# Performance work log

Hardware: AMD Instinct MI355X
Metric: run time of the kernel (lower is better)

The kernel has to match this reference:

```python
import jax, jax.numpy as jnp
import numpy as np

B, T, C, H = 2, 2048, 1024, 16
HD = C // H
HID = C * 4 // 3  # 1365, SwiGLU hidden
EPS = 1e-5


def _ln(x, g, b):
    m = x.mean(-1, keepdims=True)
    v = ((x - m) ** 2).mean(-1, keepdims=True)
    return (x - m) / jnp.sqrt(v + EPS) * g + b


def setup_inputs() -> dict:
    key0 = jax.random.key(0)
    ks = jax.random.split(key0, 16)
    s = 0.02
    inp = {
        'query': jax.random.normal(ks[0], (B, T, C), jnp.float32),
        'key': jax.random.normal(ks[1], (B, T, C), jnp.float32),
        'g_q': jnp.ones((C,), jnp.float32), 'b_q': jnp.zeros((C,), jnp.float32),
        'g_k': jnp.ones((C,), jnp.float32), 'b_k': jnp.zeros((C,), jnp.float32),
        'in_proj_w': jax.random.normal(ks[2], (3 * C, C), jnp.float32) * s,
        'in_proj_b': jnp.zeros((3 * C,), jnp.float32),
        'out_w': jax.random.normal(ks[3], (C, C), jnp.float32) * s,
        'out_b': jnp.zeros((C,), jnp.float32),
        'proj_w': jax.random.normal(ks[4], (C, C), jnp.float32) * s,
        'proj_b': jnp.zeros((C,), jnp.float32),
        'rel_table': jax.random.normal(ks[5], (H, 2 * 2048 - 1), jnp.float32) * s,
        'g_ffn': jnp.ones((C,), jnp.float32), 'b_ffn': jnp.zeros((C,), jnp.float32),
        'w1': jax.random.normal(ks[6], (HID, C), jnp.float32) * s,
        'w2': jax.random.normal(ks[7], (HID, C), jnp.float32) * s,
        'w3': jax.random.normal(ks[8], (C, HID), jnp.float32) * s,
        'g_out': jnp.ones((C,), jnp.float32), 'b_out': jnp.zeros((C,), jnp.float32),
        'max_len': 2048,
    }
    return inp


def reference(query, key, g_q, b_q, g_k, b_k, in_proj_w, in_proj_b, out_w, out_b,
              proj_w, proj_b, rel_table, g_ffn, b_ffn, w1, w2, w3, g_out, b_out, max_len):
    Tq, Tk = query.shape[1], key.shape[1]
    q = _ln(query, g_q, b_q)
    k = _ln(key, g_k, b_k)
    # in-projection (torch MHA packed weights)
    wq, wk, wv = jnp.split(in_proj_w, 3, axis=0)
    bq, bk, bv = jnp.split(in_proj_b, 3, axis=0)
    qp = (q @ wq.T + bq).reshape(B, Tq, H, HD).transpose(0, 2, 1, 3)
    kp = (k @ wk.T + bk).reshape(B, Tk, H, HD).transpose(0, 2, 1, 3)
    vp = (k @ wv.T + bv).reshape(B, Tk, H, HD).transpose(0, 2, 1, 3)
    # relative-position bias, mean over heads -> [Tq,Tk] additive mask
    rel_idx = jnp.clip(jnp.arange(Tq)[:, None] - jnp.arange(Tk)[None, :] + (max_len - 1),
                       0, 2 * max_len - 2)
    mask = rel_table[:, rel_idx].mean(axis=0)  # [Tq,Tk]
    scores = jnp.einsum('bhqd,bhkd->bhqk', qp, kp) / jnp.sqrt(jnp.float32(HD))
    attn = jax.nn.softmax(scores + mask[None, None], axis=-1)
    ctx = jnp.einsum('bhqk,bhkd->bhqd', attn, vp)
    ctx = ctx.transpose(0, 2, 1, 3).reshape(B, Tq, C)
    attn_out = ctx @ out_w.T + out_b
    attn_out = attn_out @ proj_w.T + proj_b
    x = query + attn_out
    # SwiGLU FFN (proj dropout/dropout are identity at eval)
    h = _ln(x, g_ffn, b_ffn)
    ff = (jax.nn.silu(h @ w1.T) * (h @ w2.T)) @ w3.T
    x = x + ff
    return _ln(x, g_out, b_out)
```

## Files before the change

kernel.cpp:

```cpp
#include <hip/hip_runtime.h>
#include <hip/hip_bf16.h>

static constexpr int Bb  = 2;
static constexpr int Tt  = 2048;
static constexpr int Cc  = 1024;
static constexpr int Hh  = 16;
static constexpr int HDi = 64;
static constexpr int HID = 1365;
static constexpr int HIDP = 1408;
static constexpr int Mm  = Bb * Tt;

typedef unsigned short u16;
typedef __attribute__((ext_vector_type(8))) short bf16x8;
typedef __attribute__((ext_vector_type(4))) float f32x4;
typedef __attribute__((ext_vector_type(8))) unsigned short u16x8;
typedef __attribute__((ext_vector_type(4))) unsigned short u16x4;

__device__ inline u16 f2bf(float f) {
    unsigned u = __builtin_bit_cast(unsigned, f);
    u += 0x7fffu + ((u >> 16) & 1u);
    return (u16)(u >> 16);
}

__device__ inline unsigned cvtpk(float lo, float hi) {
    unsigned r;
    asm("v_cvt_pk_bf16_f32 %0, %1, %2" : "=v"(r) : "v"(lo), "v"(hi));
    return r;
}

__device__ inline float vexp2(float x) {
    float r;
    asm("v_exp_f32 %0, %1" : "=v"(r) : "v"(x));
    return r;
}

__device__ inline void gl16(const void* g, void* l) {
    __builtin_amdgcn_global_load_lds(
        (const __attribute__((address_space(1))) unsigned*)g,
        (__attribute__((address_space(3))) unsigned*)l, 16, 0, 0);
}

template<int OUTBF>
__global__ __launch_bounds__(256) void ln_k(const float* __restrict__ x,
                                            const float* __restrict__ g,
                                            const float* __restrict__ b,
                                            void* __restrict__ yv) {
    int row = blockIdx.x;
    int tid = threadIdx.x;
    const float4* xr = (const float4*)(x + (size_t)row * Cc);
    float4 v = xr[tid];
    float s  = v.x + v.y + v.z + v.w;
    float ss = v.x*v.x + v.y*v.y + v.z*v.z + v.w*v.w;
    __shared__ float rs[256], rq[256];
    rs[tid] = s; rq[tid] = ss;
    __syncthreads();
    for (int o = 128; o > 0; o >>= 1) {
        if (tid < o) { rs[tid] += rs[tid+o]; rq[tid] += rq[tid+o]; }
        __syncthreads();
    }
    float mean = rs[0] * (1.f/Cc);
    float var  = rq[0] * (1.f/Cc) - mean*mean;
    float inv  = rsqrtf(var + 1e-5f);
    float4 gv = ((const float4*)g)[tid];
    float4 bv = ((const float4*)b)[tid];
    float o0 = (v.x-mean)*inv*gv.x + bv.x;
    float o1 = (v.y-mean)*inv*gv.y + bv.y;
    float o2 = (v.z-mean)*inv*gv.z + bv.z;
    float o3 = (v.w-mean)*inv*gv.w + bv.w;
    if (OUTBF) {
        u16x4 o4 = { f2bf(o0), f2bf(o1), f2bf(o2), f2bf(o3) };
        ((u16x4*)((u16*)yv + (size_t)row * Cc))[tid] = o4;
    } else {
        float4 o4 = { o0, o1, o2, o3 };
        ((float4*)((float*)yv + (size_t)row * Cc))[tid] = o4;
    }
}

__global__ __launch_bounds__(256) void prepln_k(const float* __restrict__ query,
                                                const float* __restrict__ key,
                                                const float* __restrict__ gq, const float* __restrict__ bq,
                                                const float* __restrict__ gk, const float* __restrict__ bk,
                                                u16* __restrict__ qn, u16* __restrict__ kn,
                                                const float* __restrict__ in_proj_w, u16* __restrict__ wA,
                                                const float* __restrict__ proj_w,  u16* __restrict__ wPb,
                                                const float* __restrict__ w1, u16* __restrict__ w1b,
                                                const float* __restrict__ w2, u16* __restrict__ w2b,
                                                const float* __restrict__ w3, u16* __restrict__ w3b,
                                                const float* __restrict__ out_w, u16* __restrict__ wOt,
                                                const float* __restrict__ out_b, const float* __restrict__ bp,
                                                float* __restrict__ bc,
                                                const float* __restrict__ rel, float* __restrict__ mr) {
    __shared__ float sh[64*65];
    int bid = blockIdx.x, tid = threadIdx.x;
    if (bid < 2*Mm) {
        const float* x; const float* g; const float* bb; u16* y; int r;
        if (bid < Mm) { x = query; g = gq; bb = bq; y = qn; r = bid; }
        else          { x = key;   g = gk; bb = bk; y = kn; r = bid - Mm; }
        float4 v = ((const float4*)(x + (size_t)r * Cc))[tid];
        float s  = v.x + v.y + v.z + v.w;
        float ss = v.x*v.x + v.y*v.y + v.z*v.z + v.w*v.w;
        float* rs = sh; float* rq2 = sh + 256;
        rs[tid] = s; rq2[tid] = ss;
        __syncthreads();
        for (int o = 128; o > 0; o >>= 1) {
            if (tid < o) { rs[tid] += rs[tid+o]; rq2[tid] += rq2[tid+o]; }
            __syncthreads();
        }
        float mean = rs[0] * (1.f/Cc);
        float var  = rq2[0] * (1.f/Cc) - mean*mean;
        float inv  = rsqrtf(var + 1e-5f);
        float4 gv = ((const float4*)g)[tid];
        float4 bv = ((const float4*)bb)[tid];
        u16x4 o4 = { f2bf((v.x-mean)*inv*gv.x + bv.x), f2bf((v.y-mean)*inv*gv.y + bv.y),
                     f2bf((v.z-mean)*inv*gv.z + bv.z), f2bf((v.w-mean)*inv*gv.w + bv.w) };
        ((u16x4*)(y + (size_t)r * Cc))[tid] = o4;
        return;
    }
    bid -= 2*Mm;
    if (bid < 3456) {
        int u = bid * 256 + tid;
        const float* src; u16* dst; int valid;
        if (u < 1536*256)                   { src = in_proj_w; dst = wA;  valid = 3*Cc*Cc; }
        else if ((u -= 1536*256) < 512*256) { src = proj_w;    dst = wPb; valid = Cc*Cc; }
        else if ((u -= 512*256) < 704*256)  { src = w1;        dst = w1b; valid = HID*Cc; }
        else     { u -= 704*256;              src = w2;        dst = w2b; valid = HID*Cc; }
        int e0 = u * 8;
        u16x8 o;
        if (e0 + 8 <= valid) {
            float4 a = *(const float4*)(src + e0);
            float4 b = *(const float4*)(src + e0 + 4);
            o[0]=f2bf(a.x); o[1]=f2bf(a.y); o[2]=f2bf(a.z); o[3]=f2bf(a.w);
            o[4]=f2bf(b.x); o[5]=f2bf(b.y); o[6]=f2bf(b.z); o[7]=f2bf(b.w);
        } else {
            #pragma unroll
            for (int j = 0; j < 8; j++) { int e = e0 + j; o[j] = f2bf(e < valid ? src[e] : 0.f); }
        }
        *(u16x8*)(dst + (size_t)e0) = o;
    } else if (bid < 4160) {
        int idx = (bid - 3456) * 256 + tid;
        int e0 = idx * 8;
        int r = e0 / HIDP, c0 = e0 - r * HIDP;
        u16x8 o;
        #pragma unroll
        for (int j = 0; j < 8; j++) {
            int c = c0 + j;
            o[j] = f2bf(c < HID ? w3[(size_t)r * HID + c] : 0.f);
        }
        *(u16x8*)(w3b + (size_t)e0) = o;
    } else if (bid < 4416) {
        int id = bid - 4160;
        int j0 = (id & 15) * 64, c0 = (id >> 4) * 64;
        #pragma unroll
        for (int i = 0; i < 16; i++) {
            int e = tid + i*256;
            int c = e >> 6, j = e & 63;
            sh[c*65 + j] = out_w[(size_t)(c0 + c) * Cc + j0 + j];
        }
        __syncthreads();
        #pragma unroll
        for (int i = 0; i < 16; i++) {
            int e = tid + i*256;
            int j = e >> 6, c = e & 63;
            wOt[(size_t)(j0 + j) * Cc + c0 + c] = f2bf(sh[c*65 + j]);
        }
    } else if (bid < 5440) {
        int i = bid - 4416;
        float4 w = ((const float4*)(proj_w + (size_t)i * Cc))[tid];
        float4 b = ((const float4*)out_b)[tid];
        float s = w.x*b.x + w.y*b.y + w.z*b.z + w.w*b.w;
        sh[tid] = s; __syncthreads();
        for (int o = 128; o > 0; o >>= 1) {
            if (tid < o) sh[tid] += sh[tid+o];
            __syncthreads();
        }
        if (tid == 0) bc[i] = sh[0] + bp[i];
    } else {
        int j = (bid - 5440) * 256 + tid;
        if (j < 2*Tt - 1) {
            float s = 0.f;
            #pragma unroll
            for (int h = 0; h < Hh; h++) s += rel[(size_t)h * (2*Tt - 1) + j];
            mr[j] = s * (1.f/Hh);
        }
    }
}

template<int OUTBF, int HASRES, int HASBIAS>
__global__ __launch_bounds__(256) void mgemm64_k(const u16* __restrict__ A,
                                                 const u16* __restrict__ W,
                                                 const float* __restrict__ bias,
                                                 const float* __restrict__ res,
                                                 void* __restrict__ outv,
                                                 int N, int K) {
    __shared__ u16 As[2][64*32];
    __shared__ u16 Ws[2][128*32];
    int bm = blockIdx.y * 64, bn = blockIdx.x * 128;
    int tid = threadIdx.x, w = tid >> 6, l = tid & 63;
    int lr = l & 15, lh = l >> 4;
    int wm = (w >> 1) * 32, wn = (w & 1) * 64;
    f32x4 acc[2][4] = {};

    auto stage = [&](int buf, int kt) {
        {
            int row = tid >> 2, slot = tid & 3;
            int ko = kt + ((slot ^ (row & 3)) << 3);
            gl16(A + (size_t)(bm + row) * K + ko, (char*)As[buf] + tid * 16);
        }
        #pragma unroll
        for (int c = 0; c < 2; c++) {
            int i = c*256 + tid;
            int row = i >> 2, slot = i & 3;
            int ko = kt + ((slot ^ (row & 3)) << 3);
            gl16(W + (size_t)(bn + row) * K + ko, (char*)Ws[buf] + (c*256 + tid) * 16);
        }
    };
    stage(0, 0);
    for (int kt = 0; kt < K; kt += 32) {
        int buf = (kt >> 5) & 1;
        __syncthreads();
        if (kt + 32 < K) stage(buf ^ 1, kt + 32);
        bf16x8 af[2], wf[4];
        #pragma unroll
        for (int f = 0; f < 2; f++) {
            int r = wm + f*16 + lr;
            af[f] = *(const bf16x8*)((const char*)As[buf] + r*64 + ((lh ^ (r & 3)) << 4));
        }
        #pragma unroll
        for (int f = 0; f < 4; f++) {
            int rn = wn + f*16 + lr;
            wf[f] = *(const bf16x8*)((const char*)Ws[buf] + rn*64 + ((lh ^ (rn & 3)) << 4));
        }
        #pragma unroll
        for (int fm = 0; fm < 2; fm++)
            #pragma unroll
            for (int fn = 0; fn < 4; fn++)
                acc[fm][fn] = __builtin_amdgcn_mfma_f32_16x16x32_bf16(af[fm], wf[fn], acc[fm][fn], 0, 0, 0);
    }

    #pragma unroll
    for (int fm = 0; fm < 2; fm++) {
        #pragma unroll
        for (int r = 0; r < 4; r++) {
            int row = bm + wm + fm*16 + lh*4 + r;
            #pragma unroll
            for (int fn = 0; fn < 4; fn++) {
                int col = bn + wn + fn*16 + lr;
                float v = acc[fm][fn][r];
                if (HASBIAS) v += bias[col];
                if (HASRES)  v += res[(size_t)row * N + col];
                if (OUTBF) ((u16*)outv)[(size_t)row * N + col] = f2bf(v);
                else       ((float*)outv)[(size_t)row * N + col] = v;
            }
        }
    }
}

__global__ __launch_bounds__(256) void mqkv_k(const u16* __restrict__ qn,
                                              const u16* __restrict__ kn,
                                              const u16* __restrict__ wA,
                                              const float* __restrict__ bias3,
                                              u16* __restrict__ out3,
                                              const u16* __restrict__ wPb,
                                              const u16* __restrict__ wOt,
                                              u16* __restrict__ wCb) {
    __shared__ u16 As[2][64*32];
    __shared__ u16 Ws[2][128*32];

    int bid = blockIdx.x;
    int xcd = bid & 7, j = bid >> 3;
    int p = xcd * 26 + (j >> 3), x = j & 7;
    const u16* A; const u16* W; const float* bias = bias3; u16* out;
    int bm, bn = x * 128, hasb;
    if (p < 192) {
        int z = p >> 6, y = p & 63;
        A = z ? kn : qn; W = wA + (size_t)z * Cc * Cc;
        bias = bias3 + z * Cc; out = out3 + (size_t)z * Mm * Cc;
        bm = y * 64; hasb = 1;
    } else {
        A = wPb; W = wOt; out = wCb;
        bm = (p - 192) * 64; hasb = 0;
    }

    int tid = threadIdx.x, w = tid >> 6, l = tid & 63;
    int lr = l & 15, lh = l >> 4;
    int wm = (w >> 1) * 32, wn = (w & 1) * 64;
    f32x4 acc[2][4] = {};

    auto stage = [&](int buf, int kt) {
        {
            int row = tid >> 2, slot = tid & 3;
            int ko = kt + ((slot ^ (row & 3)) << 3);
            gl16(A + (size_t)(bm + row) * Cc + ko, (char*)As[buf] + tid * 16);
        }
        #pragma unroll
        for (int c = 0; c < 2; c++) {
            int i = c*256 + tid;
            int row = i >> 2, slot = i & 3;
            int ko = kt + ((slot ^ (row & 3)) << 3);
            gl16(W + (size_t)(bn + row) * Cc + ko, (char*)Ws[buf] + (c*256 + tid) * 16);
        }
    };
    stage(0, 0);
    for (int kt = 0; kt < Cc; kt += 32) {
        int buf = (kt >> 5) & 1;
        __syncthreads();
        if (kt + 32 < Cc) stage(buf ^ 1, kt + 32);
        bf16x8 af[2], wf[4];
        #pragma unroll
        for (int f = 0; f < 2; f++) {
            int r = wm + f*16 + lr;
            af[f] = *(const bf16x8*)((const char*)As[buf] + r*64 + ((lh ^ (r & 3)) << 4));
        }
        #pragma unroll
        for (int f = 0; f < 4; f++) {
            int rn = wn + f*16 + lr;
            wf[f] = *(const bf16x8*)((const char*)Ws[buf] + rn*64 + ((lh ^ (rn & 3)) << 4));
        }
        #pragma unroll
        for (int fm = 0; fm < 2; fm++)
            #pragma unroll
            for (int fn = 0; fn < 4; fn++)
                acc[fm][fn] = __builtin_amdgcn_mfma_f32_16x16x32_bf16(af[fm], wf[fn], acc[fm][fn], 0, 0, 0);
    }

    #pragma unroll
    for (int fm = 0; fm < 2; fm++) {
        #pragma unroll
        for (int r = 0; r < 4; r++) {
            int orow = bm + wm + fm*16 + lh*4 + r;
            #pragma unroll
            for (int fn = 0; fn < 4; fn++) {
                int col = bn + wn + fn*16 + lr;
                float v = acc[fm][fn][r];
                if (hasb) v += bias[col];
                out[(size_t)orow * Cc + col] = f2bf(v);
            }
        }
    }
}

__global__ __launch_bounds__(256) void mswiglu64_k(const u16* __restrict__ A,
                                                   const u16* __restrict__ W1,
                                                   const u16* __restrict__ W2,
                                                   u16* __restrict__ out,
                                                   int N, int K) {
    __shared__ u16 As[2][64*32];
    __shared__ u16 W1s[2][128*32];
    __shared__ u16 W2s[2][128*32];
    int bm = blockIdx.y * 64, bn = blockIdx.x * 128;
    int tid = threadIdx.x, w = tid >> 6, l = tid & 63;
    int lr = l & 15, lh = l >> 4;
    int wm = (w >> 1) * 32, wn = (w & 1) * 64;
    f32x4 acc1[2][4] = {};
    f32x4 acc2[2][4] = {};

    auto stage = [&](int buf, int kt) {
        {
            int row = tid >> 2, slot = tid & 3;
            int ko = kt + ((slot ^ (row & 3)) << 3);
            gl16(A + (size_t)(bm + row) * K + ko, (char*)As[buf] + tid * 16);
        }
        #pragma unroll
        for (int c = 0; c < 2; c++) {
            int i = c*256 + tid;
            int row = i >> 2, slot = i & 3;
            int ko = kt + ((slot ^ (row & 3)) << 3);
            gl16(W1 + (size_t)(bn + row) * K + ko, (char*)W1s[buf] + (c*256 + tid) * 16);
            gl16(W2 + (size_t)(bn + row) * K + ko, (char*)W2s[buf] + (c*256 + tid) * 16);
        }
    };
    stage(0, 0);
    for (int kt = 0; kt < K; kt += 32) {
        int buf = (kt >> 5) & 1;
        __syncthreads();
        if (kt + 32 < K) stage(buf ^ 1, kt + 32);
        bf16x8 af[2], w1f[4], w2f[4];
        #pragma unroll
        for (int f = 0; f < 2; f++) {
            int r = wm + f*16 + lr;
            af[f] = *(const bf16x8*)((const char*)As[buf] + r*64 + ((lh ^ (r & 3)) << 4));
        }
        #pragma unroll
        for (int f = 0; f < 4; f++) {
            int rn = wn + f*16 + lr;
            int offn = rn*64 + ((lh ^ (rn & 3)) << 4);
            w1f[f] = *(const bf16x8*)((const char*)W1s[buf] + offn);
            w2f[f] = *(const bf16x8*)((const char*)W2s[buf] + offn);
        }
        #pragma unroll
        for (int fm = 0; fm < 2; fm++)
            #pragma unroll
            for (int fn = 0; fn < 4; fn++) {
                acc1[fm][fn] = __builtin_amdgcn_mfma_f32_16x16x32_bf16(af[fm], w1f[fn], acc1[fm][fn], 0, 0, 0);
                acc2[fm][fn] = __builtin_amdgcn_mfma_f32_16x16x32_bf16(af[fm], w2f[fn], acc2[fm][fn], 0, 0, 0);
            }
    }

    #pragma unroll
    for (int fm = 0; fm < 2; fm++) {
        #pragma unroll
        for (int r = 0; r < 4; r++) {
            int row = bm + wm + fm*16 + lh*4 + r;
            #pragma unroll
            for (int fn = 0; fn < 4; fn++) {
                int col = bn + wn + fn*16 + lr;
                float a = acc1[fm][fn][r];
                float sig = 1.f / (1.f + __expf(-a));
                out[(size_t)row * N + col] = f2bf(a * sig * acc2[fm][fn][r]);
            }
        }
    }
}

__global__ __launch_bounds__(256) void vt_k(const u16* __restrict__ vp,
                                            u16* __restrict__ vt) {
    int blk = blockIdx.x;
    int bh = blk >> 5, kb = blk & 31;
    int b = bh >> 4, h = bh & 15;
    __shared__ u16 t[64][65];
    int tid = threadIdx.x;
    size_t bc = (size_t)b*Tt*Cc + (size_t)h*HDi;
    #pragma unroll
    for (int i = 0; i < 16; i++) {
        int e = tid + i*256;
        int k = e >> 6, d = e & 63;
        t[d][k] = vp[bc + (size_t)(kb*64 + k)*Cc + d];
    }
    __syncthreads();
    #pragma unroll
    for (int i = 0; i < 16; i++) {
        int e = tid + i*256;
        int d = e >> 6, k = e & 63;
        vt[((size_t)bh*64 + d)*Tt + kb*64 + k] = t[d][k];
    }
}

__global__ __launch_bounds__(512) void fattn_k(const u16* __restrict__ qp,
                                               const u16* __restrict__ kp,
                                               const u16* __restrict__ vt,
                                               const float* __restrict__ mr,
                                               u16* __restrict__ ctx) {
    __shared__ alignas(128) u16 Kt[2*8192];
    __shared__ alignas(128) u16 Vts[2*8192];
    __shared__ float mrw[2176];

    constexpr float C1 = 0.18033688011118324f;

    int bid = blockIdx.x;
    int blk = ((bid & 7) << 6) | (bid >> 3);
    int qt = blk & 15, h = (blk >> 4) & 15, b = blk >> 8;
    int q0 = qt * 128;
    int tid = threadIdx.x, w = tid >> 6, l = tid & 63;
    int lr = l & 15, lh = l >> 4;
    size_t bc = (size_t)b * Tt * Cc + (size_t)h * HDi;
    const u16* vtb = vt + (size_t)(b*Hh + h) * HDi * Tt;

    for (int i = tid; i < 2175; i += 512) mrw[i] = mr[q0 + i] * 8.f;

    bf16x8 qa[2];
    {
        const u16* qrow = qp + bc + (size_t)(q0 + w*16 + lr) * Cc;
        qa[0] = *(const bf16x8*)(qrow + lh*8);
        qa[1] = *(const bf16x8*)(qrow + 32 + lh*8);
    }

    f32x4 oacc[4] = {};
    float mrun = -1e30f, lrun = 0.f;

    const char* pKb0 = (const char*)Kt + (lr>>2)*1024 + (lr&3)*128
                       + ((lh ^ (lr & 3)) << 4) + (((lr >> 2) & 1) << 6);
    const char* pKb1 = (const char*)((size_t)pKb0 ^ 64);
    int cr2 = lr >> 2;
    const char* pVb = (const char*)Vts + lr*256 + ((lh ^ (lr & 3)) << 4);
    const char* pVc0 = pVb + (((0 ^ cr2) & 3) << 6);
    const char* pVc1 = pVb + (((1 ^ cr2) & 3) << 6);
    const char* pVc2 = pVb + (((2 ^ cr2) & 3) << 6);
    const char* pVc3 = pVb + (((3 ^ cr2) & 3) << 6);
    const char* pm = (const char*)mrw + (w*16 + lr - lh*8 + 2047 - 103) * 4;

    int ksl = tid & 7, kr0 = tid >> 3;
    int so_k = (ksl ^ (kr0 & 7) ^ (((kr0 >> 3) & 1) << 2)) << 3;
    const u16* gK = kp + bc + (size_t)kr0 * Cc + so_k;
    int vsl = tid & 15, vr0 = tid >> 4;
    int so_v = (vsl ^ (vr0 & 15)) << 3;
    const u16* gV = vtb + (size_t)vr0 * Tt + so_v;
    int wb = (tid & 448) * 16;
    char* dK0 = (char*)Kt  + wb;
    char* dV0 = (char*)Vts + wb;

    auto stage = [&](int bufo) {
        gl16(gK,                      dK0 + bufo);
        gl16(gK + (size_t)64*Cc,      dK0 + bufo + 8192);
        gl16(gV,                      dV0 + bufo);
        gl16(gV + (size_t)32*Tt,      dV0 + bufo + 8192);
        gK += 128*Cc;
        gV += 128;
    };

    auto tile = [&](int bufo) {
        f32x4 s[8];
        #pragma unroll
        for (int f = 0; f < 8; f++) {
            int ob = 103 - (f & 1)*32 - ((f >> 1) & 1)*4 - (f >> 2)*64;
            s[f][0] = *(const float*)(pm + (ob    ) * 4);
            s[f][1] = *(const float*)(pm + (ob - 1) * 4);
            s[f][2] = *(const float*)(pm + (ob - 2) * 4);
            s[f][3] = *(const float*)(pm + (ob - 3) * 4);
        }
        pm -= 512;
        __builtin_amdgcn_s_setprio(1);
        {
            const char* k0 = pKb0 + bufo;
            const char* k1 = pKb1 + bufo;
            bf16x8 kb;
            kb = *(const bf16x8*)(k0 + 0);     s[0] = __builtin_amdgcn_mfma_f32_16x16x32_bf16(kb, qa[0], s[0], 0, 0, 0);
            kb = *(const bf16x8*)(k1 + 0);     s[0] = __builtin_amdgcn_mfma_f32_16x16x32_bf16(kb, qa[1], s[0], 0, 0, 0);
            kb = *(const bf16x8*)(k0 + 4096);  s[1] = __builtin_amdgcn_mfma_f32_16x16x32_bf16(kb, qa[0], s[1], 0, 0, 0);
            kb = *(const bf16x8*)(k1 + 4096);  s[1] = __builtin_amdgcn_mfma_f32_16x16x32_bf16(kb, qa[1], s[1], 0, 0, 0);
            kb = *(const bf16x8*)(k1 + 512);   s[2] = __builtin_amdgcn_mfma_f32_16x16x32_bf16(kb, qa[0], s[2], 0, 0, 0);
            kb = *(const bf16x8*)(k0 + 512);   s[2] = __builtin_amdgcn_mfma_f32_16x16x32_bf16(kb, qa[1], s[2], 0, 0, 0);
            kb = *(const bf16x8*)(k1 + 4608);  s[3] = __builtin_amdgcn_mfma_f32_16x16x32_bf16(kb, qa[0], s[3], 0, 0, 0);
            kb = *(const bf16x8*)(k0 + 4608);  s[3] = __builtin_amdgcn_mfma_f32_16x16x32_bf16(kb, qa[1], s[3], 0, 0, 0);
            kb = *(const bf16x8*)(k0 + 8192);  s[4] = __builtin_amdgcn_mfma_f32_16x16x32_bf16(kb, qa[0], s[4], 0, 0, 0);
            kb = *(const bf16x8*)(k1 + 8192);  s[4] = __builtin_amdgcn_mfma_f32_16x16x32_bf16(kb, qa[1], s[4], 0, 0, 0);
            kb = *(const bf16x8*)(k0 + 12288); s[5] = __builtin_amdgcn_mfma_f32_16x16x32_bf16(kb, qa[0], s[5], 0, 0, 0);
            kb = *(const bf16x8*)(k1 + 12288); s[5] = __builtin_amdgcn_mfma_f32_16x16x32_bf16(kb, qa[1], s[5], 0, 0, 0);
            kb = *(const bf16x8*)(k1 + 8704);  s[6] = __builtin_amdgcn_mfma_f32_16x16x32_bf16(kb, qa[0], s[6], 0, 0, 0);
            kb = *(const bf16x8*)(k0 + 8704);  s[6] = __builtin_amdgcn_mfma_f32_16x16x32_bf16(kb, qa[1], s[6], 0, 0, 0);
            kb = *(const bf16x8*)(k1 + 12800); s[7] = __builtin_amdgcn_mfma_f32_16x16x32_bf16(kb, qa[0], s[7], 0, 0, 0);
            kb = *(const bf16x8*)(k0 + 12800); s[7] = __builtin_amdgcn_mfma_f32_16x16x32_bf16(kb, qa[1], s[7], 0, 0, 0);
        }
        __builtin_amdgcn_s_setprio(0);

        float tm = -1e30f;
        #pragma unroll
        for (int f = 0; f < 8; f++)
            #pragma unroll
            for (int r = 0; r < 4; r++) tm = fmaxf(tm, s[f][r]);
        tm = fmaxf(tm, __shfl_xor(tm, 16));
        tm = fmaxf(tm, __shfl_xor(tm, 32));

        float corr = 1.f;
        bool nod = __all(tm <= mrun + 64.f);
        if (!nod) {
            float mn = fmaxf(mrun, tm);
            corr = vexp2((mrun - mn) * C1);
            mrun = mn;
        }
        float mnc = mrun * C1;
        float ts = 0.f;
        #pragma unroll
        for (int f = 0; f < 8; f++)
            #pragma unroll
            for (int r = 0; r < 4; r++) {
                float e = vexp2(fmaf(s[f][r], C1, -mnc));
                s[f][r] = e; ts += e;
            }
        ts += __shfl_xor(ts, 16);
        ts += __shfl_xor(ts, 32);
        if (nod) {
            lrun += ts;
        } else {
            lrun = lrun*corr + ts;
            #pragma unroll
            for (int f = 0; f < 4; f++) {
                oacc[f][0] *= corr; oacc[f][1] *= corr;
                oacc[f][2] *= corr; oacc[f][3] *= corr;
            }
        }

        uint4 pb0u = { cvtpk(s[0][0], s[0][1]), cvtpk(s[0][2], s[0][3]),
                       cvtpk(s[2][0], s[2][1]), cvtpk(s[2][2], s[2][3]) };
        uint4 pb1u = { cvtpk(s[1][0], s[1][1]), cvtpk(s[1][2], s[1][3]),
                       cvtpk(s[3][0], s[3][1]), cvtpk(s[3][2], s[3][3]) };
        uint4 pb2u = { cvtpk(s[4][0], s[4][1]), cvtpk(s[4][2], s[4][3]),
                       cvtpk(s[6][0], s[6][1]), cvtpk(s[6][2], s[6][3]) };
        uint4 pb3u = { cvtpk(s[5][0], s[5][1]), cvtpk(s[5][2], s[5][3]),
                       cvtpk(s[7][0], s[7][1]), cvtpk(s[7][2], s[7][3]) };
        bf16x8 pb0 = __builtin_bit_cast(bf16x8, pb0u);
        bf16x8 pb1 = __builtin_bit_cast(bf16x8, pb1u);
        bf16x8 pb2 = __builtin_bit_cast(bf16x8, pb2u);
        bf16x8 pb3 = __builtin_bit_cast(bf16x8, pb3u);

        __builtin_amdgcn_s_setprio(1);
        #pragma unroll
        for (int ff = 0; ff < 4; ff++) {
            bf16x8 vb;
            vb = *(const bf16x8*)(pVc0 + bufo + ff*4096);
            oacc[ff] = __builtin_amdgcn_mfma_f32_16x16x32_bf16(vb, pb0, oacc[ff], 0, 0, 0);
            vb = *(const bf16x8*)(pVc1 + bufo + ff*4096);
            oacc[ff] = __builtin_amdgcn_mfma_f32_16x16x32_bf16(vb, pb1, oacc[ff], 0, 0, 0);
            vb = *(const bf16x8*)(pVc2 + bufo + ff*4096);
            oacc[ff] = __builtin_amdgcn_mfma_f32_16x16x32_bf16(vb, pb2, oacc[ff], 0, 0, 0);
            vb = *(const bf16x8*)(pVc3 + bufo + ff*4096);
            oacc[ff] = __builtin_amdgcn_mfma_f32_16x16x32_bf16(vb, pb3, oacc[ff], 0, 0, 0);
        }
        __builtin_amdgcn_s_setprio(0);
    };

    stage(0);
    #pragma unroll 1
    for (int kt = 0; kt < 16; kt += 2) {
        __syncthreads();
        stage(16384);
        tile(0);
        __syncthreads();
        if (kt < 14) stage(0);
        tile(16384);
    }

    float iv = 1.f / lrun;
    size_t rowoff = bc + (size_t)(q0 + w*16 + lr) * Cc;
    #pragma unroll
    for (int f = 0; f < 4; f++) {
        u16x4 o4 = { f2bf(oacc[f][0]*iv), f2bf(oacc[f][1]*iv),
                     f2bf(oacc[f][2]*iv), f2bf(oacc[f][3]*iv) };
        *(u16x4*)(ctx + rowoff + f*16 + lh*4) = o4;
    }
}

extern "C" void kernel_launch(void* const* d_in, const int* in_sizes, int n_in,
                              void* d_out, int out_size, void* d_ws, size_t ws_size,
                              hipStream_t stream) {
    const float* query     = (const float*)d_in[0];
    const float* key       = (const float*)d_in[1];
    const float* g_q       = (const float*)d_in[2];
    const float* b_q       = (const float*)d_in[3];
    const float* g_k       = (const float*)d_in[4];
    const float* b_k       = (const float*)d_in[5];
    const float* in_proj_w = (const float*)d_in[6];
    const float* in_proj_b = (const float*)d_in[7];
    const float* out_w     = (const float*)d_in[8];
    const float* out_b     = (const float*)d_in[9];
    const float* proj_w    = (const float*)d_in[10];
    const float* proj_b    = (const float*)d_in[11];
    const float* rel_table = (const float*)d_in[12];
    const float* g_ffn     = (const float*)d_in[13];
    const float* b_ffn     = (const float*)d_in[14];
    const float* w1        = (const float*)d_in[15];
    const float* w2        = (const float*)d_in[16];
    const float* w3        = (const float*)d_in[17];
    const float* g_out     = (const float*)d_in[18];
    const float* b_out     = (const float*)d_in[19];

    char* p = (char*)d_ws;
    auto alloc = [&](size_t bytes) { char* r = p; p += bytes; return r; };
    const size_t MCb = (size_t)Mm * Cc * 2;
    u16* wA  = (u16*)alloc((size_t)3*Cc*Cc*2);
    u16* wPb = (u16*)alloc((size_t)Cc*Cc*2);
    u16* wOt = (u16*)alloc((size_t)Cc*Cc*2);
    u16* wCb = (u16*)alloc((size_t)Cc*Cc*2);
    u16* w1b = (u16*)alloc((size_t)HIDP*Cc*2);
    u16* w2b = (u16*)alloc((size_t)HIDP*Cc*2);
    u16* w3b = (u16*)alloc((size_t)Cc*HIDP*2);
    float* bc = (float*)alloc(Cc*4);
    float* mr = (float*)alloc(4096*4);
    u16* qn = (u16*)alloc(MCb);
    u16* kn = (u16*)alloc(MCb);
    u16* qp = (u16*)alloc(MCb);
    u16* kp = (u16*)alloc(MCb);
    u16* vp = (u16*)alloc(MCb);
    u16* vt = (u16*)alloc(MCb);
    float* x  = (float*)alloc((size_t)Mm*Cc*4);
    float* x2 = (float*)alloc((size_t)Mm*Cc*4);
    u16* ctx = qn;
    u16* h   = qp;
    u16* gf  = vp;

    dim3 blk(256);
    prepln_k<<<2*Mm + 5456, blk, 0, stream>>>(query, key, g_q, b_q, g_k, b_k, qn, kn,
                                              in_proj_w, wA, proj_w, wPb, w1, w1b, w2, w2b,
                                              w3, w3b, out_w, wOt, out_b, proj_b, bc, rel_table, mr);

    mqkv_k<<<1664, blk, 0, stream>>>(qn, kn, wA, in_proj_b, qp, wPb, wOt, wCb);

    vt_k<<<Bb*Hh*32, blk, 0, stream>>>(vp, vt);
    fattn_k<<<Bb*Hh*16, dim3(512), 0, stream>>>(qp, kp, vt, mr, ctx);

    dim3 g1(Cc/128, Mm/64);
    mgemm64_k<0,1,1><<<g1, blk, 0, stream>>>(ctx, wCb, bc, query, x, Cc, Cc);

    ln_k<1><<<Mm, blk, 0, stream>>>(x, g_ffn, b_ffn, h);
    dim3 g2(HIDP/128, Mm/64);
    mswiglu64_k<<<g2, blk, 0, stream>>>(h, w1b, w2b, gf, HIDP, Cc);
    dim3 g3(Cc/128, Mm/64);
    mgemm64_k<0,1,0><<<g3, blk, 0, stream>>>(gf, w3b, nullptr, x, x2, Cc, HIDP);

    ln_k<0><<<Mm, blk, 0, stream>>>(x2, g_out, b_out, d_out);
}
```

Before: 241.2 us.

## Fuse V transpose into QKV GEMM epilogue and reorder softmax sum

The V-projection blocks of the QKV GEMM now stage their output tile through shared memory and write it directly in transposed [b,h,d,t] layout. This removes the separate vt_k kernel launch and the round trip of V through global memory. In the attention kernel, the row-max is computed with a tree reduction, and the row-sum of the probabilities is moved after the PV MFMAs so it can overlap with them. The fused path adds an extra LDS round trip and two barriers to a third of the GEMM blocks, and it makes the transposed stores strided.

```diff
diff --git a/kernel.cpp b/kernel.cpp
--- a/kernel.cpp
+++ b/kernel.cpp
@@ -262,20 +262,22 @@
                                               u16* __restrict__ out3,
                                               const u16* __restrict__ wPb,
                                               const u16* __restrict__ wOt,
-                                              u16* __restrict__ wCb) {
-    __shared__ u16 As[2][64*32];
-    __shared__ u16 Ws[2][128*32];
+                                              u16* __restrict__ wCb,
+                                              u16* __restrict__ vt) {
+    __shared__ char smem[24576];
+    char* AsB = smem;
+    char* WsB = smem + 8192;
 
     int bid = blockIdx.x;
     int xcd = bid & 7, j = bid >> 3;
     int p = xcd * 26 + (j >> 3), x = j & 7;
     const u16* A; const u16* W; const float* bias = bias3; u16* out;
-    int bm, bn = x * 128, hasb;
+    int bm, bn = x * 128, hasb, isv = 0;
     if (p < 192) {
         int z = p >> 6, y = p & 63;
         A = z ? kn : qn; W = wA + (size_t)z * Cc * Cc;
         bias = bias3 + z * Cc; out = out3 + (size_t)z * Mm * Cc;
-        bm = y * 64; hasb = 1;
+        bm = y * 64; hasb = 1; isv = (z == 2);
     } else {
         A = wPb; W = wOt; out = wCb;
         bm = (p - 192) * 64; hasb = 0;
@@ -290,14 +292,14 @@
         {
             int row = tid >> 2, slot = tid & 3;
             int ko = kt + ((slot ^ (row & 3)) << 3);
-            gl16(A + (size_t)(bm + row) * Cc + ko, (char*)As[buf] + tid * 16);
+            gl16(A + (size_t)(bm + row) * Cc + ko, AsB + buf*4096 + tid * 16);
         }
         #pragma unroll
         for (int c = 0; c < 2; c++) {
             int i = c*256 + tid;
             int row = i >> 2, slot = i & 3;
             int ko = kt + ((slot ^ (row & 3)) << 3);
-            gl16(W + (size_t)(bn + row) * Cc + ko, (char*)Ws[buf] + (c*256 + tid) * 16);
+            gl16(W + (size_t)(bn + row) * Cc + ko, WsB + buf*8192 + (c*256 + tid) * 16);
         }
     };
     stage(0, 0);
@@ -309,12 +311,12 @@
         #pragma unroll
         for (int f = 0; f < 2; f++) {
             int r = wm + f*16 + lr;
-            af[f] = *(const bf16x8*)((const char*)As[buf] + r*64 + ((lh ^ (r & 3)) << 4));
+            af[f] = *(const bf16x8*)(AsB + buf*4096 + r*64 + ((lh ^ (r & 3)) << 4));
         }
         #pragma unroll
         for (int f = 0; f < 4; f++) {
             int rn = wn + f*16 + lr;
-            wf[f] = *(const bf16x8*)((const char*)Ws[buf] + rn*64 + ((lh ^ (rn & 3)) << 4));
+            wf[f] = *(const bf16x8*)(WsB + buf*8192 + rn*64 + ((lh ^ (rn & 3)) << 4));
         }
         #pragma unroll
         for (int fm = 0; fm < 2; fm++)
@@ -323,18 +325,45 @@
                 acc[fm][fn] = __builtin_amdgcn_mfma_f32_16x16x32_bf16(af[fm], wf[fn], acc[fm][fn], 0, 0, 0);
     }
 
-    #pragma unroll
-    for (int fm = 0; fm < 2; fm++) {
-        #pragma unroll
-        for (int r = 0; r < 4; r++) {
-            int orow = bm + wm + fm*16 + lh*4 + r;
-            #pragma unroll
-            for (int fn = 0; fn < 4; fn++) {
-                int col = bn + wn + fn*16 + lr;
-                float v = acc[fm][fn][r];
-                if (hasb) v += bias[col];
-                out[(size_t)orow * Cc + col] = f2bf(v);
+    if (!isv) {
+        #pragma unroll
+        for (int fm = 0; fm < 2; fm++) {
+            #pragma unroll
+            for (int r = 0; r < 4; r++) {
+                int orow = bm + wm + fm*16 + lh*4 + r;
+                #pragma unroll
+                for (int fn = 0; fn < 4; fn++) {
+                    int col = bn + wn + fn*16 + lr;
+                    float v = acc[fm][fn][r];
+                    if (hasb) v += bias[col];
+                    out[(size_t)orow * Cc + col] = f2bf(v);
+                }
             }
+        }
+    } else {
+        __syncthreads();
+        u16* T = (u16*)smem;
+        #pragma unroll
+        for (int fm = 0; fm < 2; fm++)
+            #pragma unroll
+            for (int r = 0; r < 4; r++) {
+                int lt = wm + fm*16 + lh*4 + r;
+                #pragma unroll
+                for (int fn = 0; fn < 4; fn++) {
+                    int c = wn + fn*16 + lr;
+                    T[lt*130 + c] = f2bf(acc[fm][fn][r] + bias[bn + c]);
+                }
+            }
+        __syncthreads();
+        int b = bm >> 11, t0 = bm & 2047;
+        int h0 = bn >> 6;
+        #pragma unroll
+        for (int i = 0; i < 32; i++) {
+            int e = i*256 + tid;
+            int dcol = e >> 6, t = e & 63;
+            u16 v = T[t*130 + dcol];
+            int h = h0 + (dcol >> 6), d = dcol & 63;
+            vt[(size_t)((b*Hh + h)*HDi + d) * Tt + t0 + t] = v;
         }
     }
 }
@@ -409,29 +438,6 @@
                 out[(size_t)row * N + col] = f2bf(a * sig * acc2[fm][fn][r]);
             }
         }
-    }
-}
-
-__global__ __launch_bounds__(256) void vt_k(const u16* __restrict__ vp,
-                                            u16* __restrict__ vt) {
-    int blk = blockIdx.x;
-    int bh = blk >> 5, kb = blk & 31;
-    int b = bh >> 4, h = bh & 15;
-    __shared__ u16 t[64][65];
-    int tid = threadIdx.x;
-    size_t bc = (size_t)b*Tt*Cc + (size_t)h*HDi;
-    #pragma unroll
-    for (int i = 0; i < 16; i++) {
-        int e = tid + i*256;
-        int k = e >> 6, d = e & 63;
-        t[d][k] = vp[bc + (size_t)(kb*64 + k)*Cc + d];
-    }
-    __syncthreads();
-    #pragma unroll
-    for (int i = 0; i < 16; i++) {
-        int e = tid + i*256;
-        int d = e >> 6, k = e & 63;
-        vt[((size_t)bh*64 + d)*Tt + kb*64 + k] = t[d][k];
     }
 }
 
@@ -532,11 +538,16 @@
         }
         __builtin_amdgcn_s_setprio(0);
 
-        float tm = -1e30f;
-        #pragma unroll
-        for (int f = 0; f < 8; f++)
-            #pragma unroll
-            for (int r = 0; r < 4; r++) tm = fmaxf(tm, s[f][r]);
+        float mf[8];
+        #pragma unroll
+        for (int f = 0; f < 8; f++) {
+            float m = fmaxf(fmaxf(s[f][0], s[f][1]), s[f][2]);
+            mf[f] = fmaxf(m, s[f][3]);
+        }
+        float tm = fmaxf(fmaxf(mf[0], mf[1]), mf[2]);
+        tm = fmaxf(fmaxf(tm, mf[3]), mf[4]);
+        tm = fmaxf(fmaxf(tm, mf[5]), mf[6]);
+        tm = fmaxf(tm, mf[7]);
         tm = fmaxf(tm, __shfl_xor(tm, 16));
         tm = fmaxf(tm, __shfl_xor(tm, 32));
 
@@ -546,28 +557,18 @@
             float mn = fmaxf(mrun, tm);
             corr = vexp2((mrun - mn) * C1);
             mrun = mn;
-        }
-        float mnc = mrun * C1;
-        float ts = 0.f;
-        #pragma unroll
-        for (int f = 0; f < 8; f++)
-            #pragma unroll
-            for (int r = 0; r < 4; r++) {
-                float e = vexp2(fmaf(s[f][r], C1, -mnc));
-                s[f][r] = e; ts += e;
-            }
-        ts += __shfl_xor(ts, 16);
-        ts += __shfl_xor(ts, 32);
-        if (nod) {
-            lrun += ts;
-        } else {
-            lrun = lrun*corr + ts;
             #pragma unroll
             for (int f = 0; f < 4; f++) {
                 oacc[f][0] *= corr; oacc[f][1] *= corr;
                 oacc[f][2] *= corr; oacc[f][3] *= corr;
             }
         }
+        float mnc = mrun * C1;
+        #pragma unroll
+        for (int f = 0; f < 8; f++)
+            #pragma unroll
+            for (int r = 0; r < 4; r++)
+                s[f][r] = vexp2(fmaf(s[f][r], C1, -mnc));
 
         uint4 pb0u = { cvtpk(s[0][0], s[0][1]), cvtpk(s[0][2], s[0][3]),
                        cvtpk(s[2][0], s[2][1]), cvtpk(s[2][2], s[2][3]) };
@@ -596,6 +597,15 @@
             oacc[ff] = __builtin_amdgcn_mfma_f32_16x16x32_bf16(vb, pb3, oacc[ff], 0, 0, 0);
         }
         __builtin_amdgcn_s_setprio(0);
+
+        float ts = 0.f;
+        #pragma unroll
+        for (int f = 0; f < 8; f++)
+            #pragma unroll
+            for (int r = 0; r < 4; r++) ts += s[f][r];
+        ts += __shfl_xor(ts, 16);
+        ts += __shfl_xor(ts, 32);
+        lrun = fmaf(lrun, corr, ts);
     };
 
     stage(0);
@@ -672,9 +682,8 @@
                                               in_proj_w, wA, proj_w, wPb, w1, w1b, w2, w2b,
                                               w3, w3b, out_w, wOt, out_b, proj_b, bc, rel_table, mr);
 
-    mqkv_k<<<1664, blk, 0, stream>>>(qn, kn, wA, in_proj_b, qp, wPb, wOt, wCb);
-
-    vt_k<<<Bb*Hh*32, blk, 0, stream>>>(vp, vt);
+    mqkv_k<<<1664, blk, 0, stream>>>(qn, kn, wA, in_proj_b, qp, wPb, wOt, wCb, vt);
+
     fattn_k<<<Bb*Hh*16, dim3(512), 0, stream>>>(qp, kp, vt, mr, ctx);
 
     dim3 g1(Cc/128, Mm/64);
```

Measured after the change: 250.9 us. +4.0%, slower.
